# Performance work log

Measured on AMD Instinct MI355X. Metric: run time of the kernel, lower is better.

The kernel has to match this reference:

```python
import jax, jax.numpy as jnp
import numpy as np

B, N, E = 4, 10000, 640000
IN, HID, OUT, H = 128, 64, 64, 2


def _lin(key, fi, fo):
    kw, kb = jax.random.split(key)
    w = jax.random.normal(kw, (fi, fo), dtype=jnp.float32) / np.sqrt(fi)
    b = jnp.zeros((fo,), dtype=jnp.float32)
    return w, b


def setup_inputs() -> dict:
    key = jax.random.key(0)
    ks = jax.random.split(key, 12)
    x = jax.random.normal(ks[0], (B, N, IN), dtype=jnp.float32)
    edge_index = jax.random.randint(ks[1], (2, E), 0, B * N, dtype=jnp.int64)
    # layer 1: TransformerConv(IN -> HID, heads=H, concat=False)
    Wq1, bq1 = _lin(ks[2], IN, H * HID)
    Wk1, bk1 = _lin(ks[3], IN, H * HID)
    Wv1, bv1 = _lin(ks[4], IN, H * HID)
    Ws1, bs1 = _lin(ks[5], IN, HID)  # root/skip (concat=False -> out_channels)
    # layer 2: TransformerConv(HID -> OUT, heads=H, concat=False), no activation
    Wq2, bq2 = _lin(ks[6], HID, H * OUT)
    Wk2, bk2 = _lin(ks[7], HID, H * OUT)
    Wv2, bv2 = _lin(ks[8], HID, H * OUT)
    Ws2, bs2 = _lin(ks[9], HID, OUT)
    return dict(x=x, edge_index=edge_index,
                Wq1=Wq1, bq1=bq1, Wk1=Wk1, bk1=bk1, Wv1=Wv1, bv1=bv1, Ws1=Ws1, bs1=bs1,
                Wq2=Wq2, bq2=bq2, Wk2=Wk2, bk2=bk2, Wv2=Wv2, bv2=bv2, Ws2=Ws2, bs2=bs2)


def transformer_conv(x, src, dst, Wq, bq, Wk, bk, Wv, bv, Ws, bs, heads, ch):
    """PyG TransformerConv with concat=False (mean over heads) + root skip."""
    Nn = x.shape[0]
    q = (x @ Wq + bq).reshape(Nn, heads, ch)
    k = (x @ Wk + bk).reshape(Nn, heads, ch)
    v = (x @ Wv + bv).reshape(Nn, heads, ch)
    scale = 1.0 / np.sqrt(ch)
    # edge-wise attention logits: q_i . k_j / sqrt(ch)   [E, H]
    alpha = jnp.einsum('ehc,ehc->eh', q[dst], k[src]) * scale
    # numerically stable softmax over incoming edges of each destination node
    m = jax.ops.segment_max(alpha, dst, num_segments=Nn)  # [Nn, H]
    e = jnp.exp(alpha - m[dst])
    denom = jax.ops.segment_sum(e, dst, num_segments=Nn)  # [Nn, H]
    msg = jax.ops.segment_sum(e[:, :, None] * v[src], dst, num_segments=Nn)  # [Nn,H,C]
    out = msg / jnp.maximum(denom, 1e-16)[:, :, None]
    out = out.mean(axis=1)  # concat=False -> average heads
    return out + x @ Ws + bs  # root_weight skip


def reference(x, edge_index,
              Wq1, bq1, Wk1, bk1, Wv1, bv1, Ws1, bs1,
              Wq2, bq2, Wk2, bk2, Wv2, bv2, Ws2, bs2):
    bsz, n, _ = x.shape
    xf = x.reshape(bsz * n, IN)
    src, dst = edge_index[0], edge_index[1]
    h = transformer_conv(xf, src, dst, Wq1, bq1, Wk1, bk1, Wv1, bv1, Ws1, bs1, H, HID)
    h = jax.nn.leaky_relu(h, 0.1)
    o = transformer_conv(h, src, dst, Wq2, bq2, Wk2, bk2, Wv2, bv2, Ws2, bs2, H, OUT)
    return o.reshape(bsz, n, OUT)
```

## Files before the change

kernel.cpp:

```cpp
#include <hip/hip_runtime.h>
#include <math.h>

#define NN    40000
#define HEADS 2
#define CHN   64
#define NC    448
#define KOFF  128
#define VOFF  256
#define SOFF  384

#define SCAN_BLK 256
#define NBLK ((NN + SCAN_BLK - 1) / SCAN_BLK)

__global__ void detect_k(const int* __restrict__ w, int* __restrict__ flag) {
  int lane = threadIdx.x & 63;
  int v = 0;
#pragma unroll
  for (int i = 0; i < 4; ++i) v |= w[2 * (lane + 64 * i) + 1];
#pragma unroll
  for (int o = 32; o; o >>= 1) v |= __shfl_xor(v, o);
  if (lane == 0 && blockIdx.x == 0) *flag = (v == 0) ? 1 : 0;
}

__global__ void decode_k(const int* __restrict__ w, const int* __restrict__ flag,
                         int* __restrict__ srcs, int* __restrict__ dsts,
                         int* __restrict__ deg, int E) {
  int e = blockIdx.x * blockDim.x + threadIdx.x;
  if (e >= E) return;
  int s, d;
  if (*flag) { s = w[2 * e]; d = w[2 * (E + e)]; }
  else       { s = w[e];     d = w[E + e]; }
  srcs[e] = s;
  dsts[e] = d;
  atomicAdd(&deg[d], 1);
}

__global__ void pack_all(const float* __restrict__ Wq1, const float* __restrict__ bq1,
                         const float* __restrict__ Wk1, const float* __restrict__ bk1,
                         const float* __restrict__ Wv1, const float* __restrict__ bv1,
                         const float* __restrict__ Ws1, const float* __restrict__ bs1,
                         const float* __restrict__ Wq2, const float* __restrict__ bq2,
                         const float* __restrict__ Wk2, const float* __restrict__ bk2,
                         const float* __restrict__ Wv2, const float* __restrict__ bv2,
                         const float* __restrict__ Ws2, const float* __restrict__ bs2,
                         float* __restrict__ B1, float* __restrict__ bias1,
                         float* __restrict__ B2, float* __restrict__ bias2) {
  int i = blockIdx.x * blockDim.x + threadIdx.x;
  if (i < 57344) {
    int k = i / NC, c = i % NC;
    float v;
    if (c < 128)      v = Wq1[k * 128 + c];
    else if (c < 256) v = Wk1[k * 128 + (c - 128)];
    else if (c < 384) v = Wv1[k * 128 + (c - 256)];
    else              v = Ws1[k * 64 + (c - 384)];
    B1[i] = v;
  } else if (i < 86016) {
    int j = i - 57344;
    int k = j / NC, c = j % NC;
    float v;
    if (c < 128)      v = Wq2[k * 128 + c];
    else if (c < 256) v = Wk2[k * 128 + (c - 128)];
    else if (c < 384) v = Wv2[k * 128 + (c - 256)];
    else              v = Ws2[k * 64 + (c - 384)];
    B2[j] = v;
  } else if (i < 86464) {
    int c = i - 86016;
    float v;
    if (c < 128)      v = bq1[c];
    else if (c < 256) v = bk1[c - 128];
    else if (c < 384) v = bv1[c - 256];
    else              v = bs1[c - 384];
    bias1[c] = v;
  } else if (i < 86912) {
    int c = i - 86464;
    float v;
    if (c < 128)      v = bq2[c];
    else if (c < 256) v = bk2[c - 128];
    else if (c < 384) v = bv2[c - 256];
    else              v = bs2[c - 384];
    bias2[c] = v;
  }
}

__global__ __launch_bounds__(SCAN_BLK) void bsum_k(const int* __restrict__ deg,
                                                   int* __restrict__ bsum) {
  int t = threadIdx.x;
  int i = blockIdx.x * SCAN_BLK + t;
  int v = (i < NN) ? deg[i] : 0;
#pragma unroll
  for (int o = 32; o; o >>= 1) v += __shfl_xor(v, o);
  __shared__ int ws[4];
  if ((t & 63) == 0) ws[t >> 6] = v;
  __syncthreads();
  if (t == 0) bsum[blockIdx.x] = ws[0] + ws[1] + ws[2] + ws[3];
}

__global__ __launch_bounds__(SCAN_BLK) void bscan_k(const int* __restrict__ bsum,
                                                    int* __restrict__ boff) {
  int t = threadIdx.x;
  int lane = t & 63, w = t >> 6;
  int v = (t < NBLK) ? bsum[t] : 0;
  int incl = v;
#pragma unroll
  for (int o = 1; o < 64; o <<= 1) {
    int u = __shfl_up(incl, o);
    if (lane >= o) incl += u;
  }
  __shared__ int wsum[4];
  if (lane == 63) wsum[w] = incl;
  __syncthreads();
  int woff = 0;
  for (int j = 0; j < w; ++j) woff += wsum[j];
  if (t < NBLK) boff[t] = woff + incl - v;
}

__global__ __launch_bounds__(SCAN_BLK) void rpwrite_k(const int* __restrict__ deg,
    const int* __restrict__ boff, int* __restrict__ rp, int* __restrict__ cur) {
  int t = threadIdx.x;
  int i = blockIdx.x * SCAN_BLK + t;
  int v = (i < NN) ? deg[i] : 0;
  int lane = t & 63, w = t >> 6;
  int incl = v;
#pragma unroll
  for (int o = 1; o < 64; o <<= 1) {
    int u = __shfl_up(incl, o);
    if (lane >= o) incl += u;
  }
  __shared__ int wsum[4];
  if (lane == 63) wsum[w] = incl;
  __syncthreads();
  int woff = 0;
  for (int j = 0; j < w; ++j) woff += wsum[j];
  int ex = boff[blockIdx.x] + woff + incl - v;
  if (i < NN) { rp[i] = ex; cur[i] = ex; }
  if (i == NN - 1) rp[NN] = ex + v;
}

__global__ void scatter_k(const int* __restrict__ srcs, const int* __restrict__ dsts,
                          int* __restrict__ cur, int* __restrict__ col, int E) {
  int e = blockIdx.x * blockDim.x + threadIdx.x;
  if (e < E) {
    int p = atomicAdd(&cur[dsts[e]], 1);
    col[p] = srcs[e];
  }
}

__global__ __launch_bounds__(256) void gemm_bias(const float* __restrict__ A,
    const float* __restrict__ Bm, const float* __restrict__ bias,
    float* __restrict__ C, int M, int N, int K) {
  __shared__ __align__(16) float As[32][68];
  __shared__ __align__(16) float Bs[32][64];
  int bm = blockIdx.y << 6, bn = blockIdx.x << 6;
  int tid = threadIdx.x;
  int tr = (tid >> 4) << 2;
  int tc = (tid & 15) << 2;
  float acc[4][4] = {};
  for (int k0 = 0; k0 < K; k0 += 32) {
#pragma unroll
    for (int t = 0; t < 2; ++t) {
      int i = tid + (t << 8);
      int m = i >> 3, k4 = (i & 7) << 2;
      const float4 va = *(const float4*)(A + (size_t)(bm + m) * K + k0 + k4);
      As[k4 + 0][m] = va.x; As[k4 + 1][m] = va.y;
      As[k4 + 2][m] = va.z; As[k4 + 3][m] = va.w;
      int kb = i >> 4, n4 = (i & 15) << 2;
      *(float4*)&Bs[kb][n4] = *(const float4*)(Bm + (size_t)(k0 + kb) * N + bn + n4);
    }
    __syncthreads();
#pragma unroll
    for (int kk = 0; kk < 32; ++kk) {
      const float4 av = *(const float4*)&As[kk][tr];
      const float4 bv = *(const float4*)&Bs[kk][tc];
      float a[4] = {av.x, av.y, av.z, av.w};
      float b[4] = {bv.x, bv.y, bv.z, bv.w};
#pragma unroll
      for (int i2 = 0; i2 < 4; ++i2)
#pragma unroll
        for (int j = 0; j < 4; ++j) acc[i2][j] += a[i2] * b[j];
    }
    __syncthreads();
  }
  const float4 bb = *(const float4*)&bias[bn + tc];
#pragma unroll
  for (int i2 = 0; i2 < 4; ++i2) {
    float4 o;
    o.x = acc[i2][0] + bb.x; o.y = acc[i2][1] + bb.y;
    o.z = acc[i2][2] + bb.z; o.w = acc[i2][3] + bb.w;
    *(float4*)(C + (size_t)(bm + tr + i2) * N + bn + tc) = o;
  }
}

__global__ __launch_bounds__(128) void agg_fused(const float* __restrict__ QKVS,
    const int* __restrict__ rp, const int* __restrict__ col,
    float* __restrict__ out, int act) {
  int dst = blockIdx.x;
  int h = threadIdx.x >> 6;
  int lane = threadIdx.x & 63;
  int g = lane >> 4;
  int sl = lane & 15;
  const float scale = 0.125f;

  float4 q4 = *(const float4*)(QKVS + (size_t)dst * NC + h * 64 + 4 * sl);
  q4.x *= scale; q4.y *= scale; q4.z *= scale; q4.w *= scale;
  const float* __restrict__ base = QKVS + h * 64 + 4 * sl;

  float m = -INFINITY, d = 0.f;
  float4 acc = {0.f, 0.f, 0.f, 0.f};
  int e0 = rp[dst], e1 = rp[dst + 1];

  int e = e0 + g;
  if (e < e1) {
    int sCur = col[e];
    int en = e + 4;
    int sNxt = (en < e1) ? col[en] : sCur;
    const float* rC = base + (size_t)sCur * NC;
    float4 kC = *(const float4*)(rC + KOFF);
    float4 vC = *(const float4*)(rC + VOFF);
    while (true) {
      const float* rN = base + (size_t)sNxt * NC;
      float4 kN = *(const float4*)(rN + KOFF);
      float4 vN = *(const float4*)(rN + VOFF);
      int enn = e + 8;
      int sNN = (enn < e1) ? col[enn] : sNxt;
      float p = q4.x * kC.x + q4.y * kC.y + q4.z * kC.z + q4.w * kC.w;
      p += __shfl_xor(p, 1); p += __shfl_xor(p, 2);
      p += __shfl_xor(p, 4); p += __shfl_xor(p, 8);
      float mn = fmaxf(m, p);
      float corr = __expf(m - mn);
      float w = __expf(p - mn);
      d = d * corr + w;
      acc.x = acc.x * corr + w * vC.x;
      acc.y = acc.y * corr + w * vC.y;
      acc.z = acc.z * corr + w * vC.z;
      acc.w = acc.w * corr + w * vC.w;
      m = mn;
      e += 4;
      if (e >= e1) break;
      kC = kN; vC = vN; sNxt = sNN;
    }
  }

#pragma unroll
  for (int o = 16; o <= 32; o <<= 1) {
    float m2 = __shfl_xor(m, o);
    float d2 = __shfl_xor(d, o);
    float ax = __shfl_xor(acc.x, o), ay = __shfl_xor(acc.y, o);
    float az = __shfl_xor(acc.z, o), aw = __shfl_xor(acc.w, o);
    float mn = fmaxf(m, m2);
    float c1 = __expf(fmaxf(m - mn, -88.f));
    float c2 = __expf(fmaxf(m2 - mn, -88.f));
    d = d * c1 + d2 * c2;
    acc.x = acc.x * c1 + ax * c2;
    acc.y = acc.y * c1 + ay * c2;
    acc.z = acc.z * c1 + az * c2;
    acc.w = acc.w * c1 + aw * c2;
    m = mn;
  }
  float inv = 1.0f / fmaxf(d, 1e-16f);
  float4 r = {acc.x * inv, acc.y * inv, acc.z * inv, acc.w * inv};

  __shared__ float s1[64];
  if (h == 1 && g == 0) *(float4*)&s1[4 * sl] = r;
  __syncthreads();
  if (h == 0 && g == 0) {
    const float4 rr = *(const float4*)&s1[4 * sl];
    const float4 sk = *(const float4*)(QKVS + (size_t)dst * NC + SOFF + 4 * sl);
    float4 o;
    o.x = 0.5f * (r.x + rr.x) + sk.x;
    o.y = 0.5f * (r.y + rr.y) + sk.y;
    o.z = 0.5f * (r.z + rr.z) + sk.z;
    o.w = 0.5f * (r.w + rr.w) + sk.w;
    if (act) {
      o.x = o.x > 0.f ? o.x : 0.1f * o.x;
      o.y = o.y > 0.f ? o.y : 0.1f * o.y;
      o.z = o.z > 0.f ? o.z : 0.1f * o.z;
      o.w = o.w > 0.f ? o.w : 0.1f * o.w;
    }
    *(float4*)(out + (size_t)dst * CHN + 4 * sl) = o;
  }
}

extern "C" void kernel_launch(void* const* d_in, const int* in_sizes, int n_in,
                              void* d_out, int out_size, void* d_ws, size_t ws_size,
                              hipStream_t stream) {
  const float* x = (const float*)d_in[0];
  const int* ei_raw = (const int*)d_in[1];
  const float *Wq1 = (const float*)d_in[2],  *bq1 = (const float*)d_in[3],
              *Wk1 = (const float*)d_in[4],  *bk1 = (const float*)d_in[5],
              *Wv1 = (const float*)d_in[6],  *bv1 = (const float*)d_in[7],
              *Ws1 = (const float*)d_in[8],  *bs1 = (const float*)d_in[9],
              *Wq2 = (const float*)d_in[10], *bq2 = (const float*)d_in[11],
              *Wk2 = (const float*)d_in[12], *bk2 = (const float*)d_in[13],
              *Wv2 = (const float*)d_in[14], *bv2 = (const float*)d_in[15],
              *Ws2 = (const float*)d_in[16], *bs2 = (const float*)d_in[17];
  float* out = (float*)d_out;
  const int E = in_sizes[1] / 2;

  char* base = (char*)d_ws;
  size_t off = 0;
  auto take = [&](size_t bytes) {
    char* p = base + off;
    off += (bytes + 255) & ~(size_t)255;
    return p;
  };
  float* B1    = (float*)take((size_t)128 * NC * 4);
  float* bias1 = (float*)take(NC * 4);
  float* B2    = (float*)take((size_t)64 * NC * 4);
  float* bias2 = (float*)take(NC * 4);
  int*   flag  = (int*)take(256);
  int*   deg   = (int*)take((size_t)NN * 4);
  int*   rp    = (int*)take((size_t)(NN + 1) * 4);
  int*   cur   = (int*)take((size_t)(NN + 1) * 4);
  int*   bsum  = (int*)take((size_t)NBLK * 4);
  int*   boff  = (int*)take((size_t)NBLK * 4);
  int*   srcs  = (int*)take((size_t)E * 4);
  int*   dsts  = (int*)take((size_t)E * 4);
  int*   col   = (int*)take((size_t)E * 4);
  float* QKVS  = (float*)take((size_t)NN * NC * 4);
  float* Hbuf  = (float*)take((size_t)NN * CHN * 4);
  (void)ws_size; (void)n_in; (void)out_size;

  hipMemsetAsync(deg, 0, (size_t)NN * 4, stream);
  pack_all<<<(86912 + 255) / 256, 256, 0, stream>>>(
      Wq1, bq1, Wk1, bk1, Wv1, bv1, Ws1, bs1,
      Wq2, bq2, Wk2, bk2, Wv2, bv2, Ws2, bs2, B1, bias1, B2, bias2);
  detect_k<<<1, 64, 0, stream>>>(ei_raw, flag);
  decode_k<<<(E + 255) / 256, 256, 0, stream>>>(ei_raw, flag, srcs, dsts, deg, E);
  bsum_k<<<NBLK, SCAN_BLK, 0, stream>>>(deg, bsum);
  bscan_k<<<1, SCAN_BLK, 0, stream>>>(bsum, boff);
  rpwrite_k<<<NBLK, SCAN_BLK, 0, stream>>>(deg, boff, rp, cur);
  scatter_k<<<(E + 255) / 256, 256, 0, stream>>>(srcs, dsts, cur, col, E);

  gemm_bias<<<dim3(NC / 64, NN / 64), 256, 0, stream>>>(x, B1, bias1, QKVS, NN, NC, 128);
  agg_fused<<<NN, 128, 0, stream>>>(QKVS, rp, col, Hbuf, 1);

  gemm_bias<<<dim3(NC / 64, NN / 64), 256, 0, stream>>>(Hbuf, B2, bias2, QKVS, NN, NC, 64);
  agg_fused<<<NN, 128, 0, stream>>>(QKVS, rp, col, out, 0);
}
```

Baseline: 438.3 us.

## Store K/V in bf16 interleaved layout to halve gather traffic

```diff
diff --git a/kernel.cpp b/kernel.cpp
--- a/kernel.cpp
+++ b/kernel.cpp
@@ -5,12 +5,16 @@
 #define HEADS 2
 #define CHN   64
 #define NC    448
-#define KOFF  128
-#define VOFF  256
-#define SOFF  384
+#define QSC   192
 
 #define SCAN_BLK 256
 #define NBLK ((NN + SCAN_BLK - 1) / SCAN_BLK)
+
+__device__ __forceinline__ unsigned short f2bf(float f) {
+  unsigned int u = __float_as_uint(f);
+  unsigned int r = u + 0x7fffu + ((u >> 16) & 1u);
+  return (unsigned short)(r >> 16);
+}
 
 __global__ void detect_k(const int* __restrict__ w, int* __restrict__ flag) {
   int lane = threadIdx.x & 63;
@@ -147,7 +151,7 @@
 
 __global__ __launch_bounds__(256) void gemm_bias(const float* __restrict__ A,
     const float* __restrict__ Bm, const float* __restrict__ bias,
-    float* __restrict__ C, int M, int N, int K) {
+    float* __restrict__ QS, unsigned short* __restrict__ KVH, int M, int K) {
   __shared__ __align__(16) float As[32][68];
   __shared__ __align__(16) float Bs[32][64];
   int bm = blockIdx.y << 6, bn = blockIdx.x << 6;
@@ -164,7 +168,7 @@
       As[k4 + 0][m] = va.x; As[k4 + 1][m] = va.y;
       As[k4 + 2][m] = va.z; As[k4 + 3][m] = va.w;
       int kb = i >> 4, n4 = (i & 15) << 2;
-      *(float4*)&Bs[kb][n4] = *(const float4*)(Bm + (size_t)(k0 + kb) * N + bn + n4);
+      *(float4*)&Bs[kb][n4] = *(const float4*)(Bm + (size_t)(k0 + kb) * NC + bn + n4);
     }
     __syncthreads();
 #pragma unroll
@@ -180,17 +184,32 @@
     }
     __syncthreads();
   }
-  const float4 bb = *(const float4*)&bias[bn + tc];
+  const int c0 = bn + tc;
+  const float4 bb = *(const float4*)&bias[c0];
 #pragma unroll
   for (int i2 = 0; i2 < 4; ++i2) {
+    int row = bm + tr + i2;
     float4 o;
     o.x = acc[i2][0] + bb.x; o.y = acc[i2][1] + bb.y;
     o.z = acc[i2][2] + bb.z; o.w = acc[i2][3] + bb.w;
-    *(float4*)(C + (size_t)(bm + tr + i2) * N + bn + tc) = o;
-  }
-}
-
-__global__ __launch_bounds__(128) void agg_fused(const float* __restrict__ QKVS,
+    if (c0 < 128) {
+      *(float4*)(QS + (size_t)row * QSC + c0) = o;
+    } else if (c0 < 384) {
+      int isV = (c0 >= 256);
+      int kc = c0 - 128 - (isV << 7);
+      int hh = kc >> 6, ch = kc & 63;
+      size_t off = (size_t)row * 256 + hh * 128 + (ch >> 2) * 8 + (isV << 2);
+      ushort4 w4;
+      w4.x = f2bf(o.x); w4.y = f2bf(o.y); w4.z = f2bf(o.z); w4.w = f2bf(o.w);
+      *(ushort4*)(KVH + off) = w4;
+    } else {
+      *(float4*)(QS + (size_t)row * QSC + 128 + (c0 - 384)) = o;
+    }
+  }
+}
+
+__global__ __launch_bounds__(128) void agg_fused(const float* __restrict__ QS,
+    const unsigned short* __restrict__ KVH,
     const int* __restrict__ rp, const int* __restrict__ col,
     float* __restrict__ out, int act) {
   int dst = blockIdx.x;
@@ -200,9 +219,9 @@
   int sl = lane & 15;
   const float scale = 0.125f;
 
-  float4 q4 = *(const float4*)(QKVS + (size_t)dst * NC + h * 64 + 4 * sl);
+  float4 q4 = *(const float4*)(QS + (size_t)dst * QSC + h * 64 + 4 * sl);
   q4.x *= scale; q4.y *= scale; q4.z *= scale; q4.w *= scale;
-  const float* __restrict__ base = QKVS + h * 64 + 4 * sl;
+  const unsigned short* __restrict__ kvb = KVH + h * 128 + sl * 8;
 
   float m = -INFINITY, d = 0.f;
   float4 acc = {0.f, 0.f, 0.f, 0.f};
@@ -213,30 +232,34 @@
     int sCur = col[e];
     int en = e + 4;
     int sNxt = (en < e1) ? col[en] : sCur;
-    const float* rC = base + (size_t)sCur * NC;
-    float4 kC = *(const float4*)(rC + KOFF);
-    float4 vC = *(const float4*)(rC + VOFF);
+    uint4 uC = *(const uint4*)(kvb + (size_t)sCur * 256);
     while (true) {
-      const float* rN = base + (size_t)sNxt * NC;
-      float4 kN = *(const float4*)(rN + KOFF);
-      float4 vN = *(const float4*)(rN + VOFF);
+      uint4 uN = *(const uint4*)(kvb + (size_t)sNxt * 256);
       int enn = e + 8;
       int sNN = (enn < e1) ? col[enn] : sNxt;
-      float p = q4.x * kC.x + q4.y * kC.y + q4.z * kC.z + q4.w * kC.w;
+      float k0 = __uint_as_float(uC.x << 16);
+      float k1 = __uint_as_float(uC.x & 0xffff0000u);
+      float k2 = __uint_as_float(uC.y << 16);
+      float k3 = __uint_as_float(uC.y & 0xffff0000u);
+      float p = q4.x * k0 + q4.y * k1 + q4.z * k2 + q4.w * k3;
       p += __shfl_xor(p, 1); p += __shfl_xor(p, 2);
       p += __shfl_xor(p, 4); p += __shfl_xor(p, 8);
       float mn = fmaxf(m, p);
       float corr = __expf(m - mn);
       float w = __expf(p - mn);
+      float v0 = __uint_as_float(uC.z << 16);
+      float v1 = __uint_as_float(uC.z & 0xffff0000u);
+      float v2 = __uint_as_float(uC.w << 16);
+      float v3 = __uint_as_float(uC.w & 0xffff0000u);
       d = d * corr + w;
-      acc.x = acc.x * corr + w * vC.x;
-      acc.y = acc.y * corr + w * vC.y;
-      acc.z = acc.z * corr + w * vC.z;
-      acc.w = acc.w * corr + w * vC.w;
+      acc.x = acc.x * corr + w * v0;
+      acc.y = acc.y * corr + w * v1;
+      acc.z = acc.z * corr + w * v2;
+      acc.w = acc.w * corr + w * v3;
       m = mn;
       e += 4;
       if (e >= e1) break;
-      kC = kN; vC = vN; sNxt = sNN;
+      uC = uN; sNxt = sNN;
     }
   }
 
@@ -264,7 +287,7 @@
   __syncthreads();
   if (h == 0 && g == 0) {
     const float4 rr = *(const float4*)&s1[4 * sl];
-    const float4 sk = *(const float4*)(QKVS + (size_t)dst * NC + SOFF + 4 * sl);
+    const float4 sk = *(const float4*)(QS + (size_t)dst * QSC + 128 + 4 * sl);
     float4 o;
     o.x = 0.5f * (r.x + rr.x) + sk.x;
     o.y = 0.5f * (r.y + rr.y) + sk.y;
@@ -316,7 +339,8 @@
   int*   srcs  = (int*)take((size_t)E * 4);
   int*   dsts  = (int*)take((size_t)E * 4);
   int*   col   = (int*)take((size_t)E * 4);
-  float* QKVS  = (float*)take((size_t)NN * NC * 4);
+  float* QS    = (float*)take((size_t)NN * QSC * 4);
+  unsigned short* KVH = (unsigned short*)take((size_t)NN * 256 * 2);
   float* Hbuf  = (float*)take((size_t)NN * CHN * 4);
   (void)ws_size; (void)n_in; (void)out_size;
 
@@ -331,9 +355,9 @@
   rpwrite_k<<<NBLK, SCAN_BLK, 0, stream>>>(deg, boff, rp, cur);
   scatter_k<<<(E + 255) / 256, 256, 0, stream>>>(srcs, dsts, cur, col, E);
 
-  gemm_bias<<<dim3(NC / 64, NN / 64), 256, 0, stream>>>(x, B1, bias1, QKVS, NN, NC, 128);
-  agg_fused<<<NN, 128, 0, stream>>>(QKVS, rp, col, Hbuf, 1);
-
-  gemm_bias<<<dim3(NC / 64, NN / 64), 256, 0, stream>>>(Hbuf, B2, bias2, QKVS, NN, NC, 64);
-  agg_fused<<<NN, 128, 0, stream>>>(QKVS, rp, col, out, 0);
-}
+  gemm_bias<<<dim3(NC / 64, NN / 64), 256, 0, stream>>>(x, B1, bias1, QS, KVH, NN, 128);
+  agg_fused<<<NN, 128, 0, stream>>>(QS, KVH, rp, col, Hbuf, 1);
+
+  gemm_bias<<<dim3(NC / 64, NN / 64), 256, 0, stream>>>(Hbuf, B2, bias2, QS, KVH, NN, 64);
+  agg_fused<<<NN, 128, 0, stream>>>(QS, KVH, rp, col, out, 0);
+}
```

Result: faster. 362.6 us (-17.3%).
